# Kernel optimization log

Measured on AMD Instinct MI355X. Metric: run time of the kernel, lower is better.

Reference implementation:

```python
import jax, jax.numpy as jnp
import numpy as np

TEMP = 0.07  # InfoCNECauchy temperature


def setup_inputs() -> dict:
    key = jax.random.key(0)
    k1, k2 = jax.random.split(key)
    features = jax.random.normal(k1, (8192, 512), dtype=jnp.float32)  # 2N x d, two augmented views
    labels = jax.random.randint(k2, (8192,), 0, 100)  # unused in selfsupervised mode
    return {"features": features, "labels": labels}


def reference(features, labels):
    n2 = features.shape[0]
    n = n2 // 2
    # squared pairwise Euclidean distances (== torch.cdist(...)**2)
    sq = jnp.sum(features * features, axis=1)
    d2 = jnp.maximum(sq[:, None] + sq[None, :] - 2.0 * (features @ features.T), 0.0)
    # Cauchy similarity kernel: 1 / ((dist / t)^2 + 1)
    sim = 1.0 / (d2 / (TEMP * TEMP) + 1.0)
    # selfsupervised mask: row i is positive only with its partner view i^N,
    # so the masked mean-log reduces to log(sim[i, partner(i)])
    idx = jnp.arange(n2)
    partner = jnp.where(idx < n, idx + n, idx - n)
    pos = jnp.mean(jnp.log(sim[idx, partner]))
    # negatives: sum over row excluding the diagonal (sim diag == 1)
    neg = jnp.mean(jnp.log(jnp.sum(sim, axis=1) - jnp.diagonal(sim)))
    return -(pos - neg)
```

## Files before the change

### kernel.cpp

```cpp
#include <hip/hip_runtime.h>


#define N2 8192
#define DIM 512
#define NT 64
#define NTILES (NT * (NT + 1) / 2)
#define T2 0.0049f

typedef float floatx4 __attribute__((ext_vector_type(4)));
typedef __bf16 bf16x8 __attribute__((ext_vector_type(8)));
typedef __bf16 bf16x4 __attribute__((ext_vector_type(4)));

__device__ __forceinline__ void load_to_lds16(const void* g, void* l) {
  auto gp = (const __attribute__((address_space(1))) void*)(reinterpret_cast<uintptr_t>(g));
  auto lp = (__attribute__((address_space(3))) void*)(reinterpret_cast<uintptr_t>(l));
  __builtin_amdgcn_global_load_lds(gp, lp, 16, 0, 0);
}

__global__ __launch_bounds__(256) void prep_kernel(const float* __restrict__ f,
                                                   __bf16* __restrict__ fbf,
                                                   float* __restrict__ sq,
                                                   float* __restrict__ rowsum) {
  const int t = threadIdx.x;
  if (t < 2) rowsum[blockIdx.x * 2 + t] = 0.f;
  const int row = blockIdx.x * 2 + (t >> 7);
  const int ci = (t & 127) * 4;
  const float4 v = *(const float4*)(f + (size_t)row * DIM + ci);
  bf16x4 b;
  b[0] = (__bf16)v.x; b[1] = (__bf16)v.y; b[2] = (__bf16)v.z; b[3] = (__bf16)v.w;
  *(bf16x4*)(fbf + (size_t)row * DIM + ci) = b;
  float s = v.x * v.x + v.y * v.y + v.z * v.z + v.w * v.w;
#pragma unroll
  for (int off = 1; off < 64; off <<= 1) s += __shfl_xor(s, off, 64);
  __shared__ float red[4];
  if ((t & 63) == 0) red[t >> 6] = s;
  __syncthreads();
  if ((t & 127) == 0) sq[row] = red[t >> 6] + red[(t >> 6) + 1];
}

__global__ __launch_bounds__(256) void gemm_kernel(const __bf16* __restrict__ fbf,
                                                   const float* __restrict__ sq,
                                                   float* __restrict__ rowsum,
                                                   float* __restrict__ spart) {
  __shared__ __bf16 aT[128 * 32];
  __shared__ __bf16 bT[128 * 32];

  {
    const int x = blockIdx.x & 7;
    int kk = blockIdx.x >> 3;
    int band = x;
    const int n1 = 250 - 16 * x;
    if (kk >= n1) { kk -= n1; band = 15 - x; }
    const int by0 = band * 4;
    int bxx = by0;
    int cnt;
    while (kk >= (cnt = min(4, bxx - by0 + 1))) { kk -= cnt; ++bxx; }
    __shared__ int s_by, s_bx;
    if (threadIdx.x == 0) { s_by = by0 + kk; s_bx = bxx; }
    __syncthreads();
    (void)s_by;
  }
  int by, bx;
  {
    const int x = blockIdx.x & 7;
    int kk = blockIdx.x >> 3;
    int band = x;
    const int n1 = 250 - 16 * x;
    if (kk >= n1) { kk -= n1; band = 15 - x; }
    const int by0 = band * 4;
    int bxx = by0;
    int cnt;
    while (kk >= (cnt = min(4, bxx - by0 + 1))) { kk -= cnt; ++bxx; }
    by = by0 + kk;
    bx = bxx;
  }
  const int brow = by * 128;
  const int bcol = bx * 128;
  const bool diag = (by == bx);

  const int t = threadIdx.x;
  const int lane = t & 63;
  const int w = t >> 6;
  const int wrow = (w >> 1) * 64;
  const int wcol = (w & 1) * 64;
  const int q4 = lane >> 4;
  const int lc = lane & 15;

  floatx4 acc[4][4] = {};

  int grow[2], gofs[2];
#pragma unroll
  for (int it = 0; it < 2; ++it) {
    const int slot = it * 256 + t;
    const int rp = slot >> 3;
    const int u = (slot & 7) ^ (rp & 7);
    grow[it] = rp * 2 + (u >> 2);
    gofs[it] = (u & 3) * 8;
  }

  const int up = (((lc & 1) * 4) + q4) ^ (lc >> 1);
  const int rhalf = lc >> 1;

  for (int kt = 0; kt < DIM / 32; ++kt) {
    const int k0 = kt * 32;
#pragma unroll
    for (int it = 0; it < 2; ++it) {
      load_to_lds16(fbf + (size_t)(brow + grow[it]) * DIM + k0 + gofs[it],
                    &aT[t * 8 + it * 2048]);
      load_to_lds16(fbf + (size_t)(bcol + grow[it]) * DIM + k0 + gofs[it],
                    &bT[t * 8 + it * 2048]);
    }
    __syncthreads();
    bf16x8 af[4], bfr[4];
#pragma unroll
    for (int mr = 0; mr < 4; ++mr)
      af[mr] = *(const bf16x8*)&aT[((wrow >> 1) + mr * 8 + rhalf) * 64 + up * 8];
#pragma unroll
    for (int mc = 0; mc < 4; ++mc)
      bfr[mc] = *(const bf16x8*)&bT[((wcol >> 1) + mc * 8 + rhalf) * 64 + up * 8];
#pragma unroll
    for (int mr = 0; mr < 4; ++mr)
#pragma unroll
      for (int mc = 0; mc < 4; ++mc)
        acc[mr][mc] =
            __builtin_amdgcn_mfma_f32_16x16x32_bf16(af[mr], bfr[mc], acc[mr][mc], 0, 0, 0);
    __syncthreads();
  }

  float sqc[4];
#pragma unroll
  for (int mc = 0; mc < 4; ++mc) sqc[mc] = sq[bcol + wcol + mc * 16 + lc];

  float cs[4] = {0.f, 0.f, 0.f, 0.f};

#pragma unroll
  for (int mr = 0; mr < 4; ++mr) {
#pragma unroll
    for (int reg = 0; reg < 4; ++reg) {
      const int r = brow + wrow + mr * 16 + q4 * 4 + reg;
      const float sr = sq[r];
      const int pc = r ^ (N2 / 2);
      float rs = 0.f;
#pragma unroll
      for (int mc = 0; mc < 4; ++mc) {
        const int c = bcol + wcol + mc * 16 + lc;
        const float g = acc[mr][mc][reg];
        const float d2 = fmaxf(sr + sqc[mc] - 2.f * g, 0.f);
        const float s = T2 * __builtin_amdgcn_rcpf(d2 + T2);
        if (c != r) rs += s;
        cs[mc] += s;
        if (c == pc) { spart[r] = s; spart[pc] = s; }
      }
#pragma unroll
      for (int off = 1; off < 16; off <<= 1) rs += __shfl_xor(rs, off, 64);
      if (lc == 0) atomicAdd(&rowsum[r], rs);
    }
  }

  if (!diag) {
#pragma unroll
    for (int mc = 0; mc < 4; ++mc) {
      float v = cs[mc];
      v += __shfl_xor(v, 16, 64);
      v += __shfl_xor(v, 32, 64);
      if (lane < 16) atomicAdd(&rowsum[bcol + wcol + mc * 16 + lane], v);
    }
  }
}

__global__ __launch_bounds__(256) void final_kernel(const float* __restrict__ rowsum,
                                                    const float* __restrict__ spart,
                                                    float* __restrict__ out) {
  const int t = threadIdx.x;
  float a = 0.f;
  for (int r = t; r < N2; r += 256) a += logf(rowsum[r]) - logf(spart[r]);
#pragma unroll
  for (int off = 1; off < 64; off <<= 1) a += __shfl_xor(a, off, 64);
  __shared__ float red[4];
  if ((t & 63) == 0) red[t >> 6] = a;
  __syncthreads();
  if (t == 0) out[0] = (red[0] + red[1] + red[2] + red[3]) * (1.0f / (float)N2);
}

extern "C" void kernel_launch(void* const* d_in, const int* in_sizes, int n_in,
                              void* d_out, int out_size, void* d_ws, size_t ws_size,
                              hipStream_t stream) {
  const float* features = (const float*)d_in[0];
  float* out = (float*)d_out;

  char* ws = (char*)d_ws;
  __bf16* fbf = (__bf16*)ws;
  float* sq = (float*)(ws + (size_t)N2 * DIM * sizeof(__bf16));
  float* rowsum = sq + N2;
  float* spart = rowsum + N2;

  prep_kernel<<<N2 / 2, 256, 0, stream>>>(features, fbf, sq, rowsum);
  gemm_kernel<<<NTILES, 256, 0, stream>>>(fbf, sq, rowsum, spart);
  final_kernel<<<1, 256, 0, stream>>>(rowsum, spart, out);
}
```

Measured before the change: 143.7 us.

## Switch Gram-matrix GEMM from bf16 to fp8 with scaled 16x16x128 MFMA

Features are quantized to fp8 (e4m3) in the prep kernel instead of bf16. The GEMM now uses the MI355X scaled f8f6f4 MFMA with K=128 and 128-wide K tiles, so there are 4 k-iterations instead of 16. This halves operand bytes and raises MFMA throughput, at the cost of larger quantization error in the distances. That error could noticeably change the Cauchy similarities, which are very sensitive with T=0.07. A redundant duplicate tile-index computation with an extra __syncthreads is also removed.

```diff
diff --git a/kernel.cpp b/kernel.cpp
--- a/kernel.cpp
+++ b/kernel.cpp
@@ -8,8 +8,8 @@
 #define T2 0.0049f
 
 typedef float floatx4 __attribute__((ext_vector_type(4)));
-typedef __bf16 bf16x8 __attribute__((ext_vector_type(8)));
-typedef __bf16 bf16x4 __attribute__((ext_vector_type(4)));
+typedef int intx4 __attribute__((ext_vector_type(4)));
+typedef int intx8 __attribute__((ext_vector_type(8)));
 
 __device__ __forceinline__ void load_to_lds16(const void* g, void* l) {
   auto gp = (const __attribute__((address_space(1))) void*)(reinterpret_cast<uintptr_t>(g));
@@ -18,7 +18,7 @@
 }
 
 __global__ __launch_bounds__(256) void prep_kernel(const float* __restrict__ f,
-                                                   __bf16* __restrict__ fbf,
+                                                   unsigned int* __restrict__ fq,
                                                    float* __restrict__ sq,
                                                    float* __restrict__ rowsum) {
   const int t = threadIdx.x;
@@ -26,9 +26,9 @@
   const int row = blockIdx.x * 2 + (t >> 7);
   const int ci = (t & 127) * 4;
   const float4 v = *(const float4*)(f + (size_t)row * DIM + ci);
-  bf16x4 b;
-  b[0] = (__bf16)v.x; b[1] = (__bf16)v.y; b[2] = (__bf16)v.z; b[3] = (__bf16)v.w;
-  *(bf16x4*)(fbf + (size_t)row * DIM + ci) = b;
+  int w = __builtin_amdgcn_cvt_pk_fp8_f32(v.x, v.y, 0, false);
+  w = __builtin_amdgcn_cvt_pk_fp8_f32(v.z, v.w, w, true);
+  fq[((size_t)row * DIM + ci) >> 2] = (unsigned int)w;
   float s = v.x * v.x + v.y * v.y + v.z * v.z + v.w * v.w;
 #pragma unroll
   for (int off = 1; off < 64; off <<= 1) s += __shfl_xor(s, off, 64);
@@ -38,28 +38,13 @@
   if ((t & 127) == 0) sq[row] = red[t >> 6] + red[(t >> 6) + 1];
 }
 
-__global__ __launch_bounds__(256) void gemm_kernel(const __bf16* __restrict__ fbf,
+__global__ __launch_bounds__(256) void gemm_kernel(const unsigned char* __restrict__ fq,
                                                    const float* __restrict__ sq,
                                                    float* __restrict__ rowsum,
                                                    float* __restrict__ spart) {
-  __shared__ __bf16 aT[128 * 32];
-  __shared__ __bf16 bT[128 * 32];
+  __shared__ unsigned char aT[128 * 128];
+  __shared__ unsigned char bT[128 * 128];
 
-  {
-    const int x = blockIdx.x & 7;
-    int kk = blockIdx.x >> 3;
-    int band = x;
-    const int n1 = 250 - 16 * x;
-    if (kk >= n1) { kk -= n1; band = 15 - x; }
-    const int by0 = band * 4;
-    int bxx = by0;
-    int cnt;
-    while (kk >= (cnt = min(4, bxx - by0 + 1))) { kk -= cnt; ++bxx; }
-    __shared__ int s_by, s_bx;
-    if (threadIdx.x == 0) { s_by = by0 + kk; s_bx = bxx; }
-    __syncthreads();
-    (void)s_by;
-  }
   int by, bx;
   {
     const int x = blockIdx.x & 7;
@@ -88,42 +73,48 @@
 
   floatx4 acc[4][4] = {};
 
-  int grow[2], gofs[2];
+  const unsigned char *gA[4], *gB[4];
 #pragma unroll
-  for (int it = 0; it < 2; ++it) {
-    const int slot = it * 256 + t;
-    const int rp = slot >> 3;
-    const int u = (slot & 7) ^ (rp & 7);
-    grow[it] = rp * 2 + (u >> 2);
-    gofs[it] = (u & 3) * 8;
+  for (int it = 0; it < 4; ++it) {
+    const int q = it * 256 + t;
+    const int r = q >> 3;
+    const int c = (q & 7) ^ (r & 7);
+    gA[it] = fq + (size_t)(brow + r) * DIM + c * 16;
+    gB[it] = fq + (size_t)(bcol + r) * DIM + c * 16;
   }
 
-  const int up = (((lc & 1) * 4) + q4) ^ (lc >> 1);
-  const int rhalf = lc >> 1;
+  const int c0 = (q4 * 2) ^ (lc & 7);
 
-  for (int kt = 0; kt < DIM / 32; ++kt) {
-    const int k0 = kt * 32;
+  for (int kt = 0; kt < DIM / 128; ++kt) {
 #pragma unroll
-    for (int it = 0; it < 2; ++it) {
-      load_to_lds16(fbf + (size_t)(brow + grow[it]) * DIM + k0 + gofs[it],
-                    &aT[t * 8 + it * 2048]);
-      load_to_lds16(fbf + (size_t)(bcol + grow[it]) * DIM + k0 + gofs[it],
-                    &bT[t * 8 + it * 2048]);
+    for (int it = 0; it < 4; ++it) {
+      load_to_lds16(gA[it], &aT[t * 16 + it * 4096]);
+      load_to_lds16(gB[it], &bT[t * 16 + it * 4096]);
     }
+#pragma unroll
+    for (int it = 0; it < 4; ++it) { gA[it] += 128; gB[it] += 128; }
     __syncthreads();
-    bf16x8 af[4], bfr[4];
+
+    intx8 bf[4];
 #pragma unroll
-    for (int mr = 0; mr < 4; ++mr)
-      af[mr] = *(const bf16x8*)&aT[((wrow >> 1) + mr * 8 + rhalf) * 64 + up * 8];
+    for (int mc = 0; mc < 4; ++mc) {
+      const int row = wcol + mc * 16 + lc;
+      const intx4 lo = *(const intx4*)&bT[row * 128 + c0 * 16];
+      const intx4 hi = *(const intx4*)&bT[row * 128 + (c0 ^ 1) * 16];
+      bf[mc] = __builtin_shufflevector(lo, hi, 0, 1, 2, 3, 4, 5, 6, 7);
+    }
 #pragma unroll
-    for (int mc = 0; mc < 4; ++mc)
-      bfr[mc] = *(const bf16x8*)&bT[((wcol >> 1) + mc * 8 + rhalf) * 64 + up * 8];
-#pragma unroll
-    for (int mr = 0; mr < 4; ++mr)
+    for (int mr = 0; mr < 4; ++mr) {
+      const int row = wrow + mr * 16 + lc;
+      const intx4 lo = *(const intx4*)&aT[row * 128 + c0 * 16];
+      const intx4 hi = *(const intx4*)&aT[row * 128 + (c0 ^ 1) * 16];
+      const intx8 af = __builtin_shufflevector(lo, hi, 0, 1, 2, 3, 4, 5, 6, 7);
 #pragma unroll
       for (int mc = 0; mc < 4; ++mc)
-        acc[mr][mc] =
-            __builtin_amdgcn_mfma_f32_16x16x32_bf16(af[mr], bfr[mc], acc[mr][mc], 0, 0, 0);
+        acc[mr][mc] = __builtin_amdgcn_mfma_scale_f32_16x16x128_f8f6f4(
+            af, bf[mc], acc[mr][mc], 0 , 0 ,
+            0, 127 , 0, 127 );
+    }
     __syncthreads();
   }
 
@@ -189,12 +180,12 @@
   float* out = (float*)d_out;
 
   char* ws = (char*)d_ws;
-  __bf16* fbf = (__bf16*)ws;
-  float* sq = (float*)(ws + (size_t)N2 * DIM * sizeof(__bf16));
+  unsigned int* fq = (unsigned int*)ws;
+  float* sq = (float*)(ws + (size_t)N2 * DIM);
   float* rowsum = sq + N2;
   float* spart = rowsum + N2;
 
-  prep_kernel<<<N2 / 2, 256, 0, stream>>>(features, fbf, sq, rowsum);
-  gemm_kernel<<<NTILES, 256, 0, stream>>>(fbf, sq, rowsum, spart);
+  prep_kernel<<<N2 / 2, 256, 0, stream>>>(features, fq, sq, rowsum);
+  gemm_kernel<<<NTILES, 256, 0, stream>>>((const unsigned char*)fq, sq, rowsum, spart);
   final_kernel<<<1, 256, 0, stream>>>(rowsum, spart, out);
 }
```

New measurement: 192.8 us. +34.2%, slower.

## Double-buffer LDS tiles to overlap global loads with MFMA compute

Applied to the files above, without the earlier changes.

Splits the A and B LDS tiles into two buffers each. The next K-slice is prefetched with global_load_lds while MFMAs run on the current slice, which removes one barrier per iteration and hides load latency. Global pointers are precomputed once per thread, and a duplicated tile-index computation with its own barrier is deleted. The cost is doubled LDS use per block, which may lower occupancy.

```diff
diff --git a/kernel.cpp b/kernel.cpp
--- a/kernel.cpp
+++ b/kernel.cpp
@@ -42,24 +42,9 @@
                                                    const float* __restrict__ sq,
                                                    float* __restrict__ rowsum,
                                                    float* __restrict__ spart) {
-  __shared__ __bf16 aT[128 * 32];
-  __shared__ __bf16 bT[128 * 32];
+  __shared__ __bf16 aT[2][128 * 32];
+  __shared__ __bf16 bT[2][128 * 32];
 
-  {
-    const int x = blockIdx.x & 7;
-    int kk = blockIdx.x >> 3;
-    int band = x;
-    const int n1 = 250 - 16 * x;
-    if (kk >= n1) { kk -= n1; band = 15 - x; }
-    const int by0 = band * 4;
-    int bxx = by0;
-    int cnt;
-    while (kk >= (cnt = min(4, bxx - by0 + 1))) { kk -= cnt; ++bxx; }
-    __shared__ int s_by, s_bx;
-    if (threadIdx.x == 0) { s_by = by0 + kk; s_bx = bxx; }
-    __syncthreads();
-    (void)s_by;
-  }
   int by, bx;
   {
     const int x = blockIdx.x & 7;
@@ -88,36 +73,45 @@
 
   floatx4 acc[4][4] = {};
 
-  int grow[2], gofs[2];
+  const __bf16 *gA[2], *gB[2];
 #pragma unroll
   for (int it = 0; it < 2; ++it) {
     const int slot = it * 256 + t;
     const int rp = slot >> 3;
     const int u = (slot & 7) ^ (rp & 7);
-    grow[it] = rp * 2 + (u >> 2);
-    gofs[it] = (u & 3) * 8;
+    const int gr = rp * 2 + (u >> 2);
+    const int go = (u & 3) * 8;
+    gA[it] = fbf + (size_t)(brow + gr) * DIM + go;
+    gB[it] = fbf + (size_t)(bcol + gr) * DIM + go;
   }
 
   const int up = (((lc & 1) * 4) + q4) ^ (lc >> 1);
   const int rhalf = lc >> 1;
 
+#pragma unroll
+  for (int it = 0; it < 2; ++it) {
+    load_to_lds16(gA[it], &aT[0][t * 8 + it * 2048]);
+    load_to_lds16(gB[it], &bT[0][t * 8 + it * 2048]);
+  }
+  __syncthreads();
+
   for (int kt = 0; kt < DIM / 32; ++kt) {
-    const int k0 = kt * 32;
+    const int cur = kt & 1;
+    if (kt + 1 < DIM / 32) {
+      const int k0 = (kt + 1) * 32;
 #pragma unroll
-    for (int it = 0; it < 2; ++it) {
-      load_to_lds16(fbf + (size_t)(brow + grow[it]) * DIM + k0 + gofs[it],
-                    &aT[t * 8 + it * 2048]);
-      load_to_lds16(fbf + (size_t)(bcol + grow[it]) * DIM + k0 + gofs[it],
-                    &bT[t * 8 + it * 2048]);
+      for (int it = 0; it < 2; ++it) {
+        load_to_lds16(gA[it] + k0, &aT[cur ^ 1][t * 8 + it * 2048]);
+        load_to_lds16(gB[it] + k0, &bT[cur ^ 1][t * 8 + it * 2048]);
+      }
     }
-    __syncthreads();
     bf16x8 af[4], bfr[4];
 #pragma unroll
     for (int mr = 0; mr < 4; ++mr)
-      af[mr] = *(const bf16x8*)&aT[((wrow >> 1) + mr * 8 + rhalf) * 64 + up * 8];
+      af[mr] = *(const bf16x8*)&aT[cur][((wrow >> 1) + mr * 8 + rhalf) * 64 + up * 8];
 #pragma unroll
     for (int mc = 0; mc < 4; ++mc)
-      bfr[mc] = *(const bf16x8*)&bT[((wcol >> 1) + mc * 8 + rhalf) * 64 + up * 8];
+      bfr[mc] = *(const bf16x8*)&bT[cur][((wcol >> 1) + mc * 8 + rhalf) * 64 + up * 8];
 #pragma unroll
     for (int mr = 0; mr < 4; ++mr)
 #pragma unroll
```

Result: slower. 156.4 us (+8.8%).
